# Performance work log

Hardware: AMD Instinct MI355X
Metric: run time of the kernel (lower is better)

The kernel has to match this reference:

```python
import jax, jax.numpy as jnp
import numpy as np

MARGIN = 0.5  # stands in for c.embedding_loss['margin']


def setup_inputs() -> dict:
    key = jax.random.key(0)
    k1, k2 = jax.random.split(key)
    emb = jax.random.normal(k1, (4, 64, 64, 64), dtype=jnp.float32)  # Bs x Ch x W x H
    lab = jax.random.randint(k2, (4, 64, 64), 0, 10)                 # Bs x W x H int labels
    return {"emb": emb, "lab": lab}


def reference(emb, lab):
    bs, ch, w, h = emb.shape
    N = h * w
    # Faithful to torch: input[i].view(h*w, ch) is a raw row-major reshape of [ch,w,h]
    E = emb.reshape(bs, N, ch)                     # [B, N, C]
    sim = jnp.einsum('bnc,bmc->bnm', E, E)         # cosine-sim-style Gram matrix [B,N,N]

    labf = lab.reshape(bs, N)
    same = labf[:, :, None] == labf[:, None, :]    # [B,N,N] bool; label_pair==+1 where same

    # pre-weight: 1 / (#pixels with same label) per pixel; count via pairwise equality
    counts = jnp.sum(same, axis=-1).astype(emb.dtype)   # [B,N]
    pw = 1.0 / counts
    weight = pw[:, :, None] * pw[:, None, :]            # [B,N,N] outer product per batch

    # positive pairs: 1 - sim ; negative pairs: relu(sim - margin)
    per_pair = jnp.where(same, 1.0 - sim, jnp.maximum(sim - MARGIN, 0.0))

    S = jnp.sum(weight * per_pair, axis=(1, 2))         # [B]
    # Original assigns the per-batch scalar (1/N)*S_i to an NxN tensor then sums everything:
    # total = sum_i N^2 * (1/N) * S_i = N * sum_i S_i
    return jnp.asarray(N, emb.dtype) * jnp.sum(S)
```

## Files before the change

kernel.cpp:

```cpp
#include <hip/hip_runtime.h>
#include <hip/hip_bf16.h>

#define NB    4
#define NPIX  4096
#define CH    64
#define TILE  128
#define TPB   32
#define PAIRS 528
#define MARGIN 0.5f
#define NCLS  10

typedef __attribute__((ext_vector_type(8))) short   bf16x8;
typedef __attribute__((ext_vector_type(4))) float   f32x4;
typedef __attribute__((ext_vector_type(4))) int     i32x4;

static __device__ inline int cvt_pk_bf16(float lo, float hi) {
    int r;
    asm("v_cvt_pk_bf16_f32 %0, %1, %2" : "=v"(r) : "v"(lo), "v"(hi));
    return r;
}

__launch_bounds__(256)
__global__ void pair_kernel(const float* __restrict__ emb, const int* __restrict__ lab,
                            float* __restrict__ partials) {
    __shared__ short As[TILE * CH];
    __shared__ short Bs[TILE * CH];
    __shared__ int   rlab[TILE], clab[TILE];
    __shared__ float rpw[TILE], cpw[TILE];
    __shared__ int   histw[4][NCLS];
    __shared__ float wred[4];

    const int bid = blockIdx.x;
    const int b   = bid / PAIRS;
    int p = bid - b * PAIRS;
    int ti = 0, off = 0;
    while (p >= off + (TPB - ti)) { off += TPB - ti; ++ti; }
    const int tj = ti + (p - off);
    const int rowbase = ti * TILE, colbase = tj * TILE;

    const float* Eb = emb + (size_t)b * NPIX * CH;
    const int*   Lb = lab + b * NPIX;
    const int t = threadIdx.x;
    const int lane = t & 63, wid = t >> 6;

    if (t < TILE) rlab[t] = Lb[rowbase + t];
    else          clab[t - TILE] = Lb[colbase + (t - TILE)];

    {
        int cnt = 0;
        const int* base = Lb + wid * 1024 + lane;
#pragma unroll
        for (int it = 0; it < 16; ++it) {
            const int lv = base[it * 64];
#pragma unroll
            for (int c = 0; c < NCLS; ++c) {
                unsigned long long m = __ballot(lv == c);
                if (lane == c) cnt += (int)__popcll(m);
            }
        }
        if (lane < NCLS) histw[wid][lane] = cnt;
    }

    {
        const int row  = t >> 1;
        const int half = t & 1;
        const float* srcA = Eb + (size_t)(rowbase + row) * CH + half * 32;
        const float* srcB = Eb + (size_t)(colbase + row) * CH + half * 32;
        char* AsB = (char*)As;
        char* BsB = (char*)Bs;
        const int sw = (row & 7) << 4;
#pragma unroll
        for (int j = 0; j < 4; ++j) {
            const int boff = row * 128 + ((half * 64 + j * 16) ^ sw);
            {
                f32x4 x0 = *(const f32x4*)(srcA + j * 8);
                f32x4 x1 = *(const f32x4*)(srcA + j * 8 + 4);
                i32x4 v = { cvt_pk_bf16(x0[0], x0[1]), cvt_pk_bf16(x0[2], x0[3]),
                            cvt_pk_bf16(x1[0], x1[1]), cvt_pk_bf16(x1[2], x1[3]) };
                *(i32x4*)(AsB + boff) = v;
            }
            {
                f32x4 x0 = *(const f32x4*)(srcB + j * 8);
                f32x4 x1 = *(const f32x4*)(srcB + j * 8 + 4);
                i32x4 v = { cvt_pk_bf16(x0[0], x0[1]), cvt_pk_bf16(x0[2], x0[3]),
                            cvt_pk_bf16(x1[0], x1[1]), cvt_pk_bf16(x1[2], x1[3]) };
                *(i32x4*)(BsB + boff) = v;
            }
        }
    }
    __syncthreads();

    if (t < TILE) {
        const int c = rlab[t];
        rpw[t] = 1.0f / (float)(histw[0][c] + histw[1][c] + histw[2][c] + histw[3][c]);
    } else {
        const int u = t - TILE;
        const int c = clab[u];
        cpw[u] = 1.0f / (float)(histw[0][c] + histw[1][c] + histw[2][c] + histw[3][c]);
    }

    const int wr = wid >> 1, wc = wid & 1;
    const int lrow = lane & 15, lk = lane >> 4;

    f32x4 acc[4][4];
#pragma unroll
    for (int i = 0; i < 4; ++i)
#pragma unroll
        for (int j = 0; j < 4; ++j) acc[i][j] = (f32x4){0.f, 0.f, 0.f, 0.f};

    const char* AsB = (const char*)As;
    const char* BsB = (const char*)Bs;
#pragma unroll
    for (int kk = 0; kk < 2; ++kk) {
        bf16x8 af[4], bfv[4];
#pragma unroll
        for (int i = 0; i < 4; ++i) {
            const int row = wr * 64 + i * 16 + lrow;
            af[i] = *(const bf16x8*)(AsB + row * 128 + ((kk * 64 + lk * 16) ^ ((row & 7) << 4)));
        }
#pragma unroll
        for (int j = 0; j < 4; ++j) {
            const int row = wc * 64 + j * 16 + lrow;
            bfv[j] = *(const bf16x8*)(BsB + row * 128 + ((kk * 64 + lk * 16) ^ ((row & 7) << 4)));
        }
#pragma unroll
        for (int i = 0; i < 4; ++i)
#pragma unroll
            for (int j = 0; j < 4; ++j)
                acc[i][j] = __builtin_amdgcn_mfma_f32_16x16x32_bf16(af[i], bfv[j], acc[i][j], 0, 0, 0);
    }
    __syncthreads();

    float facc = 0.f;
#pragma unroll
    for (int j = 0; j < 4; ++j) {
        const int c = wc * 64 + j * 16 + lrow;
        const int cl = clab[c];
        const float cp = cpw[c];
#pragma unroll
        for (int i = 0; i < 4; ++i) {
#pragma unroll
            for (int r = 0; r < 4; ++r) {
                const int rr = wr * 64 + i * 16 + lk * 4 + r;
                const float sim = acc[i][j][r];
                const float val = (rlab[rr] == cl) ? (1.0f - sim)
                                                   : fmaxf(sim - MARGIN, 0.0f);
                facc = fmaf(rpw[rr] * cp, val, facc);
            }
        }
    }

#pragma unroll
    for (int o = 32; o > 0; o >>= 1) facc += __shfl_down(facc, o);
    if (lane == 0) wred[wid] = facc;
    __syncthreads();
    if (t == 0) {
        float s = wred[0] + wred[1] + wred[2] + wred[3];
        partials[bid] = s * ((ti == tj) ? 1.0f : 2.0f);
    }
}

__global__ void reduce_kernel(const float* __restrict__ partials, float* __restrict__ out, int n) {
    float s = 0.f;
    for (int i = threadIdx.x; i < n; i += 256) s += partials[i];
#pragma unroll
    for (int o = 32; o > 0; o >>= 1) s += __shfl_down(s, o);
    __shared__ float wred[4];
    if ((threadIdx.x & 63) == 0) wred[threadIdx.x >> 6] = s;
    __syncthreads();
    if (threadIdx.x == 0) out[0] = (wred[0] + wred[1] + wred[2] + wred[3]) * (float)NPIX;
}

extern "C" void kernel_launch(void* const* d_in, const int* in_sizes, int n_in,
                              void* d_out, int out_size, void* d_ws, size_t ws_size,
                              hipStream_t stream) {
    const float* emb = (const float*)d_in[0];
    const int*   lab = (const int*)d_in[1];
    float* out = (float*)d_out;
    float* partials = (float*)d_ws;

    pair_kernel<<<NB * PAIRS, 256, 0, stream>>>(emb, lab, partials);
    reduce_kernel<<<1, 256, 0, stream>>>(partials, out, NB * PAIRS);
}
```

Measured before the change: 104.0 us.

## Precompute bf16 swizzled embeddings and class counts in prep kernel, atomically reduce

Adds a prep kernel that converts the embeddings once into a pre-swizzled bf16 workspace and computes per-batch inverse class counts. Before this, each of the 2112 tile blocks recomputed its own label histogram and converted fp32 to bf16 itself. The pair kernel now copies bf16 rows straight into LDS and looks up the weights, which halves its global load bytes and removes the redundant histogram work. The final reduce kernel is replaced by float atomicAdd into the output, which the prep kernel zeroes. This makes the summation order nondeterministic and adds a dependent launch.

```diff
diff --git a/kernel.cpp b/kernel.cpp
--- a/kernel.cpp
+++ b/kernel.cpp
@@ -9,6 +9,7 @@
 #define PAIRS 528
 #define MARGIN 0.5f
 #define NCLS  10
+#define ROWB  128
 
 typedef __attribute__((ext_vector_type(8))) short   bf16x8;
 typedef __attribute__((ext_vector_type(4))) float   f32x4;
@@ -20,14 +21,61 @@
     return r;
 }
 
+#define WS_INVCNT_OFF (NB * NPIX * ROWB)
+
+__global__ void prep_kernel(const float* __restrict__ emb, const int* __restrict__ lab,
+                            unsigned char* __restrict__ wsbf, float* __restrict__ invcnt,
+                            float* __restrict__ out) {
+    __shared__ int histw[4][NCLS];
+    const int t = threadIdx.x, blk = blockIdx.x;
+
+    const int g0 = (blk * 256 + t) * 2;
+#pragma unroll
+    for (int u = 0; u < 2; ++u) {
+        const int g   = g0 + u;
+        const int b   = g >> 15;
+        const int rem = g & 32767;
+        const int row = rem >> 3;
+        const int ci  = rem & 7;
+        const float* src = emb + ((size_t)(b * NPIX + row)) * CH + ci * 8;
+        f32x4 x0 = *(const f32x4*)src;
+        f32x4 x1 = *(const f32x4*)(src + 4);
+        i32x4 v = { cvt_pk_bf16(x0[0], x0[1]), cvt_pk_bf16(x0[2], x0[3]),
+                    cvt_pk_bf16(x1[0], x1[1]), cvt_pk_bf16(x1[2], x1[3]) };
+        *(i32x4*)(wsbf + (size_t)(b * NPIX + row) * ROWB + ((ci ^ (row & 7)) * 16)) = v;
+    }
+
+    if (blk < NB) {
+        const int lane = t & 63, wid = t >> 6;
+        int cnt = 0;
+        const int* base = lab + blk * NPIX + wid * 1024 + lane;
+#pragma unroll
+        for (int it = 0; it < 16; ++it) {
+            const int lv = base[it * 64];
+#pragma unroll
+            for (int c = 0; c < NCLS; ++c) {
+                unsigned long long m = __ballot(lv == c);
+                if (lane == c) cnt += (int)__popcll(m);
+            }
+        }
+        if (lane < NCLS) histw[wid][lane] = cnt;
+        __syncthreads();
+        if (t < NCLS)
+            invcnt[blk * 16 + t] =
+                1.0f / (float)(histw[0][t] + histw[1][t] + histw[2][t] + histw[3][t]);
+    }
+
+    if (blk == NB && t == 0) out[0] = 0.0f;
+}
+
 __launch_bounds__(256)
-__global__ void pair_kernel(const float* __restrict__ emb, const int* __restrict__ lab,
-                            float* __restrict__ partials) {
+__global__ void pair_kernel(const unsigned char* __restrict__ wsbf, const int* __restrict__ lab,
+                            const float* __restrict__ invcnt, float* __restrict__ out) {
     __shared__ short As[TILE * CH];
     __shared__ short Bs[TILE * CH];
     __shared__ int   rlab[TILE], clab[TILE];
     __shared__ float rpw[TILE], cpw[TILE];
-    __shared__ int   histw[4][NCLS];
+    __shared__ float invc[16];
     __shared__ float wred[4];
 
     const int bid = blockIdx.x;
@@ -38,66 +86,29 @@
     const int tj = ti + (p - off);
     const int rowbase = ti * TILE, colbase = tj * TILE;
 
-    const float* Eb = emb + (size_t)b * NPIX * CH;
-    const int*   Lb = lab + b * NPIX;
     const int t = threadIdx.x;
     const int lane = t & 63, wid = t >> 6;
 
-    if (t < TILE) rlab[t] = Lb[rowbase + t];
-    else          clab[t - TILE] = Lb[colbase + (t - TILE)];
+    if (t < 16) invc[t] = invcnt[b * 16 + t];
+    if (t < TILE) rlab[t] = lab[b * NPIX + rowbase + t];
+    else          clab[t - TILE] = lab[b * NPIX + colbase + (t - TILE)];
 
     {
-        int cnt = 0;
-        const int* base = Lb + wid * 1024 + lane;
-#pragma unroll
-        for (int it = 0; it < 16; ++it) {
-            const int lv = base[it * 64];
-#pragma unroll
-            for (int c = 0; c < NCLS; ++c) {
-                unsigned long long m = __ballot(lv == c);
-                if (lane == c) cnt += (int)__popcll(m);
-            }
-        }
-        if (lane < NCLS) histw[wid][lane] = cnt;
-    }
-
-    {
-        const int row  = t >> 1;
-        const int half = t & 1;
-        const float* srcA = Eb + (size_t)(rowbase + row) * CH + half * 32;
-        const float* srcB = Eb + (size_t)(colbase + row) * CH + half * 32;
+        const unsigned char* srcA = wsbf + (size_t)(b * NPIX + rowbase) * ROWB;
+        const unsigned char* srcB = wsbf + (size_t)(b * NPIX + colbase) * ROWB;
         char* AsB = (char*)As;
         char* BsB = (char*)Bs;
-        const int sw = (row & 7) << 4;
 #pragma unroll
-        for (int j = 0; j < 4; ++j) {
-            const int boff = row * 128 + ((half * 64 + j * 16) ^ sw);
-            {
-                f32x4 x0 = *(const f32x4*)(srcA + j * 8);
-                f32x4 x1 = *(const f32x4*)(srcA + j * 8 + 4);
-                i32x4 v = { cvt_pk_bf16(x0[0], x0[1]), cvt_pk_bf16(x0[2], x0[3]),
-                            cvt_pk_bf16(x1[0], x1[1]), cvt_pk_bf16(x1[2], x1[3]) };
-                *(i32x4*)(AsB + boff) = v;
-            }
-            {
-                f32x4 x0 = *(const f32x4*)(srcB + j * 8);
-                f32x4 x1 = *(const f32x4*)(srcB + j * 8 + 4);
-                i32x4 v = { cvt_pk_bf16(x0[0], x0[1]), cvt_pk_bf16(x0[2], x0[3]),
-                            cvt_pk_bf16(x1[0], x1[1]), cvt_pk_bf16(x1[2], x1[3]) };
-                *(i32x4*)(BsB + boff) = v;
-            }
+        for (int rd = 0; rd < 4; ++rd) {
+            const int o = rd * 4096 + t * 16;
+            *(i32x4*)(AsB + o) = *(const i32x4*)(srcA + o);
+            *(i32x4*)(BsB + o) = *(const i32x4*)(srcB + o);
         }
     }
     __syncthreads();
 
-    if (t < TILE) {
-        const int c = rlab[t];
-        rpw[t] = 1.0f / (float)(histw[0][c] + histw[1][c] + histw[2][c] + histw[3][c]);
-    } else {
-        const int u = t - TILE;
-        const int c = clab[u];
-        cpw[u] = 1.0f / (float)(histw[0][c] + histw[1][c] + histw[2][c] + histw[3][c]);
-    }
+    if (t < TILE) rpw[t] = invc[rlab[t]];
+    else          cpw[t - TILE] = invc[clab[t - TILE]];
 
     const int wr = wid >> 1, wc = wid & 1;
     const int lrow = lane & 15, lk = lane >> 4;
@@ -156,19 +167,9 @@
     __syncthreads();
     if (t == 0) {
         float s = wred[0] + wred[1] + wred[2] + wred[3];
-        partials[bid] = s * ((ti == tj) ? 1.0f : 2.0f);
+        s *= ((ti == tj) ? 1.0f : 2.0f) * (float)NPIX;
+        atomicAdd(out, s);
     }
-}
-
-__global__ void reduce_kernel(const float* __restrict__ partials, float* __restrict__ out, int n) {
-    float s = 0.f;
-    for (int i = threadIdx.x; i < n; i += 256) s += partials[i];
-#pragma unroll
-    for (int o = 32; o > 0; o >>= 1) s += __shfl_down(s, o);
-    __shared__ float wred[4];
-    if ((threadIdx.x & 63) == 0) wred[threadIdx.x >> 6] = s;
-    __syncthreads();
-    if (threadIdx.x == 0) out[0] = (wred[0] + wred[1] + wred[2] + wred[3]) * (float)NPIX;
 }
 
 extern "C" void kernel_launch(void* const* d_in, const int* in_sizes, int n_in,
@@ -177,8 +178,9 @@
     const float* emb = (const float*)d_in[0];
     const int*   lab = (const int*)d_in[1];
     float* out = (float*)d_out;
-    float* partials = (float*)d_ws;
+    unsigned char* wsbf = (unsigned char*)d_ws;
+    float* invcnt = (float*)((char*)d_ws + WS_INVCNT_OFF);
 
-    pair_kernel<<<NB * PAIRS, 256, 0, stream>>>(emb, lab, partials);
-    reduce_kernel<<<1, 256, 0, stream>>>(partials, out, NB * PAIRS);
+    prep_kernel<<<256, 256, 0, stream>>>(emb, lab, wsbf, invcnt, out);
+    pair_kernel<<<NB * PAIRS, 256, 0, stream>>>(wsbf, lab, invcnt, out);
 }
```

New measurement: 93.10 us. -10.5%, faster.

## Hoist label histogram into prep kernel and reduce partials via atomics

Applied to the files above, without the earlier changes.

Moves the per-batch class histogram and inverse-count computation out of every pair block into a small prep kernel run once per batch. Each pair block now loads a 16-entry inverse-count table instead of scanning 4096 labels with ballots. It also replaces the partials buffer and separate reduce kernel with a float atomicAdd into the output, which the prep kernel zeroes. The cost is an extra kernel launch in front of the pair kernel, plus contention on a single atomic and a summation order that is no longer deterministic.

```diff
diff --git a/kernel.cpp b/kernel.cpp
--- a/kernel.cpp
+++ b/kernel.cpp
@@ -20,14 +20,38 @@
     return r;
 }
 
+__global__ void prep_kernel(const int* __restrict__ lab, float* __restrict__ invcnt,
+                            float* __restrict__ out) {
+    __shared__ int histw[4][NCLS];
+    const int t = threadIdx.x, b = blockIdx.x;
+    const int lane = t & 63, wid = t >> 6;
+    int cnt = 0;
+    const int* base = lab + b * NPIX + wid * 1024 + lane;
+#pragma unroll
+    for (int it = 0; it < 16; ++it) {
+        const int lv = base[it * 64];
+#pragma unroll
+        for (int c = 0; c < NCLS; ++c) {
+            unsigned long long m = __ballot(lv == c);
+            if (lane == c) cnt += (int)__popcll(m);
+        }
+    }
+    if (lane < NCLS) histw[wid][lane] = cnt;
+    __syncthreads();
+    if (t < NCLS)
+        invcnt[b * 16 + t] =
+            1.0f / (float)(histw[0][t] + histw[1][t] + histw[2][t] + histw[3][t]);
+    if (b == 0 && t == 0) out[0] = 0.0f;
+}
+
 __launch_bounds__(256)
 __global__ void pair_kernel(const float* __restrict__ emb, const int* __restrict__ lab,
-                            float* __restrict__ partials) {
+                            const float* __restrict__ invcnt, float* __restrict__ out) {
     __shared__ short As[TILE * CH];
     __shared__ short Bs[TILE * CH];
     __shared__ int   rlab[TILE], clab[TILE];
     __shared__ float rpw[TILE], cpw[TILE];
-    __shared__ int   histw[4][NCLS];
+    __shared__ float invc[16];
     __shared__ float wred[4];
 
     const int bid = blockIdx.x;
@@ -39,27 +63,12 @@
     const int rowbase = ti * TILE, colbase = tj * TILE;
 
     const float* Eb = emb + (size_t)b * NPIX * CH;
-    const int*   Lb = lab + b * NPIX;
     const int t = threadIdx.x;
     const int lane = t & 63, wid = t >> 6;
 
-    if (t < TILE) rlab[t] = Lb[rowbase + t];
-    else          clab[t - TILE] = Lb[colbase + (t - TILE)];
-
-    {
-        int cnt = 0;
-        const int* base = Lb + wid * 1024 + lane;
-#pragma unroll
-        for (int it = 0; it < 16; ++it) {
-            const int lv = base[it * 64];
-#pragma unroll
-            for (int c = 0; c < NCLS; ++c) {
-                unsigned long long m = __ballot(lv == c);
-                if (lane == c) cnt += (int)__popcll(m);
-            }
-        }
-        if (lane < NCLS) histw[wid][lane] = cnt;
-    }
+    if (t < 16) invc[t] = invcnt[b * 16 + t];
+    if (t < TILE) rlab[t] = lab[b * NPIX + rowbase + t];
+    else          clab[t - TILE] = lab[b * NPIX + colbase + (t - TILE)];
 
     {
         const int row  = t >> 1;
@@ -90,14 +99,8 @@
     }
     __syncthreads();
 
-    if (t < TILE) {
-        const int c = rlab[t];
-        rpw[t] = 1.0f / (float)(histw[0][c] + histw[1][c] + histw[2][c] + histw[3][c]);
-    } else {
-        const int u = t - TILE;
-        const int c = clab[u];
-        cpw[u] = 1.0f / (float)(histw[0][c] + histw[1][c] + histw[2][c] + histw[3][c]);
-    }
+    if (t < TILE) rpw[t] = invc[rlab[t]];
+    else          cpw[t - TILE] = invc[clab[t - TILE]];
 
     const int wr = wid >> 1, wc = wid & 1;
     const int lrow = lane & 15, lk = lane >> 4;
@@ -156,19 +159,9 @@
     __syncthreads();
     if (t == 0) {
         float s = wred[0] + wred[1] + wred[2] + wred[3];
-        partials[bid] = s * ((ti == tj) ? 1.0f : 2.0f);
+        s *= ((ti == tj) ? 1.0f : 2.0f) * (float)NPIX;
+        atomicAdd(out, s);
     }
-}
-
-__global__ void reduce_kernel(const float* __restrict__ partials, float* __restrict__ out, int n) {
-    float s = 0.f;
-    for (int i = threadIdx.x; i < n; i += 256) s += partials[i];
-#pragma unroll
-    for (int o = 32; o > 0; o >>= 1) s += __shfl_down(s, o);
-    __shared__ float wred[4];
-    if ((threadIdx.x & 63) == 0) wred[threadIdx.x >> 6] = s;
-    __syncthreads();
-    if (threadIdx.x == 0) out[0] = (wred[0] + wred[1] + wred[2] + wred[3]) * (float)NPIX;
 }
 
 extern "C" void kernel_launch(void* const* d_in, const int* in_sizes, int n_in,
@@ -177,8 +170,8 @@
     const float* emb = (const float*)d_in[0];
     const int*   lab = (const int*)d_in[1];
     float* out = (float*)d_out;
-    float* partials = (float*)d_ws;
+    float* invcnt = (float*)d_ws;
 
-    pair_kernel<<<NB * PAIRS, 256, 0, stream>>>(emb, lab, partials);
-    reduce_kernel<<<1, 256, 0, stream>>>(partials, out, NB * PAIRS);
+    prep_kernel<<<NB, 256, 0, stream>>>(lab, invcnt, out);
+    pair_kernel<<<NB * PAIRS, 256, 0, stream>>>(emb, lab, invcnt, out);
 }
```

Result: faster. 96.11 us (-7.6%).
